# Kernel optimization log

Measured on AMD Instinct MI355X. Metric: run time of the kernel, lower is better.

Reference implementation:

```python
import jax, jax.numpy as jnp
import numpy as np

B, D, U1, U2 = 16384, 512, 512, 512
BN_EPS = 1e-3  # keras BatchNormalization default epsilon


def sparsemax(z):
    # z: [..., D]; standard sparsemax along last axis (Martins & Astudillo)
    d = z.shape[-1]
    z_sorted = -jnp.sort(-z, axis=-1)                      # descending
    z_cum = jnp.cumsum(z_sorted, axis=-1)
    k = jnp.arange(1, d + 1, dtype=z.dtype)
    support = (1.0 + k * z_sorted) > z_cum                 # [..., D] bool
    k_z = jnp.sum(support, axis=-1, keepdims=True)         # support size
    tau = (jnp.take_along_axis(z_cum, k_z.astype(jnp.int32) - 1, axis=-1) - 1.0) / k_z.astype(z.dtype)
    return jnp.maximum(z - tau, 0.0)


def setup_inputs() -> dict:
    key = jax.random.key(0)
    ks = jax.random.split(key, 8)
    x = jax.random.normal(ks[0], (B, D), dtype=jnp.float32)
    W1 = jax.random.normal(ks[1], (D, U1), dtype=jnp.float32) * 0.05
    b1 = jnp.zeros((U1,), jnp.float32)
    centers = jax.random.normal(ks[2], (U2, D), dtype=jnp.float32)      # paraboloid centers
    coefs = jax.random.normal(ks[3], (U2, D), dtype=jnp.float32) * 0.1  # paraboloid axis coefficients
    bn_gamma = jnp.ones((D,), jnp.float32)
    bn_beta = jnp.zeros((D,), jnp.float32)
    bn_mean = jnp.zeros((D,), jnp.float32)
    bn_var = jnp.ones((D,), jnp.float32)
    W_out = jax.random.normal(ks[4], (U1 + U2, D), dtype=jnp.float32) * 0.05
    b_out = jnp.zeros((D,), jnp.float32)
    w_add = jnp.array([0.5, 0.5], jnp.float32)  # WeightedAdd learnable scalars
    return {"x": x, "W1": W1, "b1": b1, "centers": centers, "coefs": coefs,
            "bn_gamma": bn_gamma, "bn_beta": bn_beta, "bn_mean": bn_mean, "bn_var": bn_var,
            "W_out": W_out, "b_out": b_out, "w_add": w_add}


def reference(x, W1, b1, centers, coefs, bn_gamma, bn_beta, bn_mean, bn_var, W_out, b_out, w_add):
    # Dense branch
    h1 = jax.nn.relu(x @ W1 + b1)                               # [B, U1]
    # BoundedParaboloids branch: BatchNorm (inference stats) then bounded paraboloids
    xb = (x - bn_mean) * jax.lax.rsqrt(bn_var + BN_EPS) * bn_gamma + bn_beta
    # q_j = sum_d (coefs[j,d] * (xb_d - centers[j,d]))^2, computed via GEMMs
    A = coefs * coefs                                            # [U2, D]
    q = (xb * xb) @ A.T - 2.0 * (xb @ (A * centers).T) + jnp.sum(A * centers * centers, axis=-1)
    h2 = jax.nn.relu(1.0 - q)                                    # [B, U2] bounded paraboloids
    # Output embedding: Dense(relu) on concat
    emb = jax.nn.relu(jnp.concatenate([h1, h2], axis=-1) @ W_out + b_out)  # [B, D]
    # WeightedAdd of (dropout-identity) inputs and embedding; dropout_rate=0 / inference
    pre = w_add[0] * x + w_add[1] * emb
    mask = sparsemax(pre)                                        # [B, D]
    return mask
```

## Files before the change

kernel.cpp:

```cpp
#include <hip/hip_runtime.h>
#include <math.h>

typedef float f4 __attribute__((ext_vector_type(4)));
typedef float f32x4 __attribute__((ext_vector_type(4)));
typedef __bf16 bf16x8 __attribute__((ext_vector_type(8)));
typedef unsigned short u16;
typedef u16 us8 __attribute__((ext_vector_type(8)));

__device__ __forceinline__ u16 f2bf(float f) {
  unsigned u = __builtin_bit_cast(unsigned, f);
  unsigned r = u + 0x7fffu + ((u >> 16) & 1u);
  return (u16)(r >> 16);
}
__device__ __forceinline__ float bf2f(u16 h) {
  unsigned u = ((unsigned)h) << 16;
  return __builtin_bit_cast(float, u);
}

__global__ __launch_bounds__(256) void prep_bn_kernel(
    const float* __restrict__ gamma, const float* __restrict__ beta,
    const float* __restrict__ mean, const float* __restrict__ var,
    float* __restrict__ scale, float* __restrict__ shift) {
  int d = blockIdx.x * blockDim.x + threadIdx.x;
  if (d < 512) {
    float s = rsqrtf(var[d] + 1e-3f) * gamma[d];
    scale[d] = s;
    shift[d] = beta[d] - mean[d] * s;
  }
}

__global__ __launch_bounds__(64) void prep_params_kernel(
    const float* __restrict__ coefs, const float* __restrict__ centers,
    u16* __restrict__ pth, float* __restrict__ cvec) {
  int j = blockIdx.x;
  int l = threadIdx.x;
  int d0 = l * 8;
  f4 c0 = *(const f4*)(coefs + (size_t)j * 512 + d0);
  f4 c1 = *(const f4*)(coefs + (size_t)j * 512 + d0 + 4);
  f4 e0 = *(const f4*)(centers + (size_t)j * 512 + d0);
  f4 e1 = *(const f4*)(centers + (size_t)j * 512 + d0 + 4);
  us8 pa, pb;
  float acc = 0.f;
#pragma unroll
  for (int e = 0; e < 8; ++e) {
    float cf = (e < 4) ? c0[e] : c1[e - 4];
    float ce = (e < 4) ? e0[e] : e1[e - 4];
    float a = cf * cf;
    pa[e] = f2bf(a);
    pb[e] = f2bf(-2.f * a * ce);
    acc = fmaf(a * ce, ce, acc);
  }
  *(us8*)(pth + (size_t)j * 1024 + d0) = pa;
  *(us8*)(pth + (size_t)j * 1024 + 512 + d0) = pb;
#pragma unroll
  for (int off = 32; off; off >>= 1) acc += __shfl_xor(acc, off);
  if (l == 0) cvec[j] = acc;
}

__global__ __launch_bounds__(256) void transpose_split_kernel(
    const float* __restrict__ in, u16* __restrict__ th, u16* __restrict__ tl,
    int K, int N) {
  __shared__ float t[32][33];
  int lx = threadIdx.x;
  int ly = threadIdx.y;
  int n0 = blockIdx.x * 32, k0 = blockIdx.y * 32;
#pragma unroll
  for (int i = 0; i < 4; ++i)
    t[ly + 8 * i][lx] = in[(size_t)(k0 + ly + 8 * i) * N + n0 + lx];
  __syncthreads();
#pragma unroll
  for (int i = 0; i < 4; ++i) {
    float v = t[lx][ly + 8 * i];
    u16 h = f2bf(v);
    u16 lo = f2bf(v - bf2f(h));
    th[(size_t)(n0 + ly + 8 * i) * K + k0 + lx] = h;
    tl[(size_t)(n0 + ly + 8 * i) * K + k0 + lx] = lo;
  }
}

__global__ __launch_bounds__(256) void conv_x_kernel(
    const float* __restrict__ x, const float* __restrict__ scale,
    const float* __restrict__ shift, u16* __restrict__ xh,
    u16* __restrict__ xb) {
  int gid = blockIdx.x * 256 + threadIdx.x;
  int m = gid >> 6;
  int d0 = (gid & 63) * 8;
  f4 v0 = *(const f4*)(x + (size_t)m * 512 + d0);
  f4 v1 = *(const f4*)(x + (size_t)m * 512 + d0 + 4);
  f4 s0 = *(const f4*)(scale + d0);
  f4 s1 = *(const f4*)(scale + d0 + 4);
  f4 h0 = *(const f4*)(shift + d0);
  f4 h1 = *(const f4*)(shift + d0 + 4);
  us8 oh, ob;
#pragma unroll
  for (int e = 0; e < 8; ++e) {
    float xv = (e < 4) ? v0[e] : v1[e - 4];
    float sc = (e < 4) ? s0[e] : s1[e - 4];
    float sh = (e < 4) ? h0[e] : h1[e - 4];
    oh[e] = f2bf(xv);
    ob[e] = f2bf(fmaf(xv, sc, sh));
  }
  *(us8*)(xh + (size_t)m * 512 + d0) = oh;
  *(us8*)(xb + (size_t)m * 512 + d0) = ob;
}

template <int MODE, int PASSES>
__global__ __launch_bounds__(256, 2) void gemm_mfma(
    const u16* __restrict__ Ah, const u16* __restrict__ Bh,
    const u16* __restrict__ Bl, const float* __restrict__ bias,
    const float* __restrict__ xorig, const float* __restrict__ wadd,
    u16* __restrict__ Hout, float* __restrict__ outp, int K, int lda,
    int coff) {
  extern __shared__ char smem[];
  char* sA = smem;
  char* sBh = smem + 16384;
  char* sBl = smem + 32768;
  const int tid = threadIdx.x;
  const int l = tid & 63;
  const int w = tid >> 6;
  const int wm = w & 1, wn = w >> 1;
  const int lr = l & 15, lk = l >> 4;
  const int sx = lr & 7;
  const int bid = blockIdx.x;
  const int lin = (bid & 7) * 64 + (bid >> 3);
  const int m0 = (lin >> 2) * 128, n0 = (lin & 3) * 128;
  const int srow = l >> 3;
  const int sslot = (l & 7) ^ srow;

  f32x4 acc[4][4];
#pragma unroll
  for (int i = 0; i < 4; ++i)
#pragma unroll
    for (int j = 0; j < 4; ++j) acc[i][j] = (f32x4){0.f, 0.f, 0.f, 0.f};

  for (int k0 = 0; k0 < K; k0 += 64) {
#pragma unroll
    for (int p = 0; p < 4; ++p) {
      int c = p * 4 + w;
      int row = c * 8 + srow;
      int loff = c * 1024;
      size_t gob = (size_t)(n0 + row) * K + k0 + sslot * 8;
      __builtin_amdgcn_global_load_lds(
          (const __attribute__((address_space(1))) void*)(Bh + gob),
          (__attribute__((address_space(3))) void*)(sBh + loff), 16, 0, 0);
      if (PASSES == 2) {
        __builtin_amdgcn_global_load_lds(
            (const __attribute__((address_space(1))) void*)(Bl + gob),
            (__attribute__((address_space(3))) void*)(sBl + loff), 16, 0, 0);
      }
      if (MODE == 2) {
        int kb = (k0 < 512) ? k0 : (k0 - 512);
        us8 v = *(const us8*)(Ah + (size_t)(m0 + row) * 512 + kb + sslot * 8);
        us8 o;
        if (k0 < 512) {
#pragma unroll
          for (int e = 0; e < 8; ++e) {
            float f = bf2f(v[e]);
            o[e] = f2bf(f * f);
          }
        } else {
          o = v;
        }
        *(us8*)(sA + loff + l * 16) = o;
      } else {
        size_t goa = (size_t)(m0 + row) * lda + k0 + sslot * 8;
        __builtin_amdgcn_global_load_lds(
            (const __attribute__((address_space(1))) void*)(Ah + goa),
            (__attribute__((address_space(3))) void*)(sA + loff), 16, 0, 0);
      }
    }
    __syncthreads();
#pragma unroll
    for (int ks = 0; ks < 2; ++ks) {
      bf16x8 av[4], bv[4];
#pragma unroll
      for (int i = 0; i < 4; ++i)
        av[i] = *(const bf16x8*)(sA + (wm * 64 + i * 16 + lr) * 128 +
                                 (((ks * 4 + lk) ^ sx) * 16));
#pragma unroll
      for (int j = 0; j < 4; ++j)
        bv[j] = *(const bf16x8*)(sBh + (wn * 64 + j * 16 + lr) * 128 +
                                 (((ks * 4 + lk) ^ sx) * 16));
#pragma unroll
      for (int i = 0; i < 4; ++i)
#pragma unroll
        for (int j = 0; j < 4; ++j)
          acc[i][j] = __builtin_amdgcn_mfma_f32_16x16x32_bf16(av[i], bv[j],
                                                              acc[i][j], 0, 0, 0);
      if (PASSES == 2) {
#pragma unroll
        for (int j = 0; j < 4; ++j)
          bv[j] = *(const bf16x8*)(sBl + (wn * 64 + j * 16 + lr) * 128 +
                                   (((ks * 4 + lk) ^ sx) * 16));
#pragma unroll
        for (int i = 0; i < 4; ++i)
#pragma unroll
          for (int j = 0; j < 4; ++j)
            acc[i][j] = __builtin_amdgcn_mfma_f32_16x16x32_bf16(
                av[i], bv[j], acc[i][j], 0, 0, 0);
      }
    }
    __syncthreads();
  }

  const int mwb = m0 + wm * 64;
  const int nwb = n0 + wn * 64;
  if (MODE == 3) {
    float w0 = wadd[0], w1 = wadd[1];
#pragma unroll
    for (int j = 0; j < 4; ++j) {
      int n = nwb + j * 16 + lr;
      float bv = bias[n];
#pragma unroll
      for (int i = 0; i < 4; ++i) {
#pragma unroll
        for (int r = 0; r < 4; ++r) {
          int m = mwb + i * 16 + lk * 4 + r;
          float v = fmaxf(acc[i][j][r] + bv, 0.f);
          outp[(size_t)m * 512 + n] =
              fmaf(w1, v, w0 * xorig[(size_t)m * 512 + n]);
        }
      }
    }
  } else {
#pragma unroll
    for (int j = 0; j < 4; ++j) {
      int n = nwb + j * 16 + lr;
      float bv = bias[n];
#pragma unroll
      for (int i = 0; i < 4; ++i) {
#pragma unroll
        for (int r = 0; r < 4; ++r) {
          int m = mwb + i * 16 + lk * 4 + r;
          float v = acc[i][j][r] + bv;
          v = (MODE == 1) ? fmaxf(v, 0.f) : fmaxf(1.f - v, 0.f);
          Hout[(size_t)m * 1024 + coff + n] = f2bf(v);
        }
      }
    }
  }
}

__global__ __launch_bounds__(256) void sparsemax_kernel(float* __restrict__ out) {
  int row = blockIdx.x * 4 + (threadIdx.x >> 6);
  int lane = threadIdx.x & 63;
  float* rp = out + (size_t)row * 512;
  f4 z0 = *(const f4*)(rp + lane * 8);
  f4 z1 = *(const f4*)(rp + lane * 8 + 4);
  float z[8];
#pragma unroll
  for (int e = 0; e < 4; ++e) {
    z[e] = z0[e];
    z[4 + e] = z1[e];
  }
  float m = z[0];
#pragma unroll
  for (int i = 1; i < 8; ++i) m = fmaxf(m, z[i]);
#pragma unroll
  for (int off = 32; off; off >>= 1) m = fmaxf(m, __shfl_xor(m, off));
  float tau = m - 1.0f;
  for (int it = 0; it < 32; ++it) {
    float s = 0.f, k = 0.f;
#pragma unroll
    for (int i = 0; i < 8; ++i) {
      if (z[i] > tau) {
        s += z[i] - tau;
        k += 1.f;
      }
    }
#pragma unroll
    for (int off = 32; off; off >>= 1) {
      s += __shfl_xor(s, off);
      k += __shfl_xor(k, off);
    }
    if (k < 0.5f) break;
    float tn = tau + (s - 1.f) / k;
    if (tn == tau) break;
    tau = tn;
  }
  float s = 0.f, k = 0.f;
#pragma unroll
  for (int i = 0; i < 8; ++i)
    if (z[i] > tau) {
      s += z[i];
      k += 1.f;
    }
#pragma unroll
  for (int off = 32; off; off >>= 1) {
    s += __shfl_xor(s, off);
    k += __shfl_xor(k, off);
  }
  float tauf = (k >= 0.5f) ? (s - 1.f) / k : (m - 1.f);
  f4 o0, o1;
#pragma unroll
  for (int e = 0; e < 4; ++e) {
    o0[e] = fmaxf(z[e] - tauf, 0.f);
    o1[e] = fmaxf(z[4 + e] - tauf, 0.f);
  }
  *(f4*)(rp + lane * 8) = o0;
  *(f4*)(rp + lane * 8 + 4) = o1;
}

extern "C" void kernel_launch(void* const* d_in, const int* in_sizes, int n_in,
                              void* d_out, int out_size, void* d_ws,
                              size_t ws_size, hipStream_t stream) {
  const float* x = (const float*)d_in[0];
  const float* W1 = (const float*)d_in[1];
  const float* b1 = (const float*)d_in[2];
  const float* centers = (const float*)d_in[3];
  const float* coefs = (const float*)d_in[4];
  const float* gamma = (const float*)d_in[5];
  const float* beta = (const float*)d_in[6];
  const float* mean = (const float*)d_in[7];
  const float* var = (const float*)d_in[8];
  const float* W_out = (const float*)d_in[9];
  const float* b_out = (const float*)d_in[10];
  const float* wadd = (const float*)d_in[11];
  float* out = (float*)d_out;

  char* ws = (char*)d_ws;
  u16* Hh = (u16*)(ws);
  u16* Xh = (u16*)(ws + 33554432);
  u16* Xb = (u16*)(ws + 50331648);
  char* pool = ws + 67108864;
  u16* W1th = (u16*)(pool);
  u16* W1tl = (u16*)(pool + 524288);
  u16* Pth = (u16*)(pool + 1048576);
  u16* Wth = (u16*)(pool);
  u16* Wtl = (u16*)(pool + 1048576);
  float* cvec = (float*)(ws + 69206016);
  float* scale = (float*)(ws + 69208064);
  float* shift = (float*)(ws + 69210112);

  prep_bn_kernel<<<2, 256, 0, stream>>>(gamma, beta, mean, var, scale, shift);
  prep_params_kernel<<<512, 64, 0, stream>>>(coefs, centers, Pth, cvec);
  transpose_split_kernel<<<dim3(16, 16), dim3(32, 8), 0, stream>>>(W1, W1th,
                                                                   W1tl, 512,
                                                                   512);
  conv_x_kernel<<<4096, 256, 0, stream>>>(x, scale, shift, Xh, Xb);

  gemm_mfma<1, 1><<<512, 256, 32768, stream>>>(Xh, W1th, nullptr, b1, nullptr,
                                               nullptr, Hh, nullptr, 512, 512,
                                               0);
  gemm_mfma<2, 1><<<512, 256, 32768, stream>>>(Xb, Pth, nullptr, cvec,
                                               nullptr, nullptr, Hh, nullptr,
                                               1024, 512, 512);
  transpose_split_kernel<<<dim3(16, 32), dim3(32, 8), 0, stream>>>(W_out, Wth,
                                                                   Wtl, 1024,
                                                                   512);
  gemm_mfma<3, 2><<<512, 256, 49152, stream>>>(Hh, Wth, Wtl, b_out, x, wadd,
                                               nullptr, out, 1024, 1024, 0);
  sparsemax_kernel<<<4096, 256, 0, stream>>>(out);
}
```

Baseline: 128.1 us.

## Fuse dense and paraboloid GEMMs into one launch; drop lo pass for h2

The two first-stage GEMMs (dense branch with K=512 and paraboloid branch with K=1024) now run as a single launch of 1024 blocks. Each block picks its branch from its block index, and the occupancy hint is raised to 4 blocks per CU. This removes one launch and its tail and lets both branches fill the GPU together. The output GEMM also now applies the bf16 hi/lo split of W_out only for the first 512 K entries (the h1 half), cutting matrix-core work and LDS traffic, at some cost in precision on the h2 contribution.

```diff
diff --git a/kernel.cpp b/kernel.cpp
--- a/kernel.cpp
+++ b/kernel.cpp
@@ -104,13 +104,116 @@
   *(us8*)(xb + (size_t)m * 512 + d0) = ob;
 }
 
-template <int MODE, int PASSES>
-__global__ __launch_bounds__(256, 2) void gemm_mfma(
+__global__ __launch_bounds__(256, 4) void gemm_fused12(
+    const u16* __restrict__ Xh, const u16* __restrict__ Xb,
+    const u16* __restrict__ W1th, const u16* __restrict__ Pth,
+    const float* __restrict__ b1, const float* __restrict__ cvec,
+    u16* __restrict__ Hout) {
+  extern __shared__ char smem[];
+  char* sA = smem;
+  char* sBh = smem + 16384;
+  const int tid = threadIdx.x;
+  const int l = tid & 63;
+  const int w = tid >> 6;
+  const int wm = w & 1, wn = w >> 1;
+  const int lr = l & 15, lk = l >> 4;
+  const int sx = lr & 7;
+  const int bid = blockIdx.x;
+  const int L = (bid & 7) * 128 + (bid >> 3);
+  const int p = L >> 3;
+  const int g = (L >> 2) & 1;
+  const int n = L & 3;
+  const int m0 = p * 128, n0 = n * 128;
+  const int Kg = g ? 1024 : 512;
+  const u16* Bmat = g ? Pth : W1th;
+  const u16* Amat = g ? Xb : Xh;
+  const int srow = l >> 3;
+  const int sslot = (l & 7) ^ srow;
+
+  f32x4 acc[4][4];
+#pragma unroll
+  for (int i = 0; i < 4; ++i)
+#pragma unroll
+    for (int j = 0; j < 4; ++j) acc[i][j] = (f32x4){0.f, 0.f, 0.f, 0.f};
+
+  for (int k0 = 0; k0 < Kg; k0 += 64) {
+#pragma unroll
+    for (int pp = 0; pp < 4; ++pp) {
+      int c = pp * 4 + w;
+      int row = c * 8 + srow;
+      int loff = c * 1024;
+      size_t gob = (size_t)(n0 + row) * Kg + k0 + sslot * 8;
+      __builtin_amdgcn_global_load_lds(
+          (const __attribute__((address_space(1))) void*)(Bmat + gob),
+          (__attribute__((address_space(3))) void*)(sBh + loff), 16, 0, 0);
+      if (g) {
+        int kb = (k0 < 512) ? k0 : (k0 - 512);
+        us8 v = *(const us8*)(Amat + (size_t)(m0 + row) * 512 + kb + sslot * 8);
+        us8 o;
+        if (k0 < 512) {
+#pragma unroll
+          for (int e = 0; e < 8; ++e) {
+            float f = bf2f(v[e]);
+            o[e] = f2bf(f * f);
+          }
+        } else {
+          o = v;
+        }
+        *(us8*)(sA + loff + l * 16) = o;
+      } else {
+        size_t goa = (size_t)(m0 + row) * 512 + k0 + sslot * 8;
+        __builtin_amdgcn_global_load_lds(
+            (const __attribute__((address_space(1))) void*)(Amat + goa),
+            (__attribute__((address_space(3))) void*)(sA + loff), 16, 0, 0);
+      }
+    }
+    __syncthreads();
+#pragma unroll
+    for (int ks = 0; ks < 2; ++ks) {
+      bf16x8 av[4], bv[4];
+#pragma unroll
+      for (int i = 0; i < 4; ++i)
+        av[i] = *(const bf16x8*)(sA + (wm * 64 + i * 16 + lr) * 128 +
+                                 (((ks * 4 + lk) ^ sx) * 16));
+#pragma unroll
+      for (int j = 0; j < 4; ++j)
+        bv[j] = *(const bf16x8*)(sBh + (wn * 64 + j * 16 + lr) * 128 +
+                                 (((ks * 4 + lk) ^ sx) * 16));
+#pragma unroll
+      for (int i = 0; i < 4; ++i)
+#pragma unroll
+        for (int j = 0; j < 4; ++j)
+          acc[i][j] = __builtin_amdgcn_mfma_f32_16x16x32_bf16(av[i], bv[j],
+                                                              acc[i][j], 0, 0, 0);
+    }
+    __syncthreads();
+  }
+
+  const int mwb = m0 + wm * 64;
+  const int nwb = n0 + wn * 64;
+  const float* bias = g ? cvec : b1;
+#pragma unroll
+  for (int j = 0; j < 4; ++j) {
+    int nn = nwb + j * 16 + lr;
+    float bv = bias[nn];
+#pragma unroll
+    for (int i = 0; i < 4; ++i) {
+#pragma unroll
+      for (int r = 0; r < 4; ++r) {
+        int m = mwb + i * 16 + lk * 4 + r;
+        float v = acc[i][j][r] + bv;
+        v = g ? fmaxf(1.f - v, 0.f) : fmaxf(v, 0.f);
+        Hout[(size_t)m * 1024 + g * 512 + nn] = f2bf(v);
+      }
+    }
+  }
+}
+
+__global__ __launch_bounds__(256, 2) void gemm3(
     const u16* __restrict__ Ah, const u16* __restrict__ Bh,
     const u16* __restrict__ Bl, const float* __restrict__ bias,
     const float* __restrict__ xorig, const float* __restrict__ wadd,
-    u16* __restrict__ Hout, float* __restrict__ outp, int K, int lda,
-    int coff) {
+    float* __restrict__ outp) {
   extern __shared__ char smem[];
   char* sA = smem;
   char* sBh = smem + 16384;
@@ -133,41 +236,26 @@
 #pragma unroll
     for (int j = 0; j < 4; ++j) acc[i][j] = (f32x4){0.f, 0.f, 0.f, 0.f};
 
-  for (int k0 = 0; k0 < K; k0 += 64) {
-#pragma unroll
-    for (int p = 0; p < 4; ++p) {
-      int c = p * 4 + w;
+  for (int k0 = 0; k0 < 1024; k0 += 64) {
+    const bool lo = (k0 < 512);
+#pragma unroll
+    for (int pp = 0; pp < 4; ++pp) {
+      int c = pp * 4 + w;
       int row = c * 8 + srow;
       int loff = c * 1024;
-      size_t gob = (size_t)(n0 + row) * K + k0 + sslot * 8;
+      size_t gob = (size_t)(n0 + row) * 1024 + k0 + sslot * 8;
+      size_t goa = (size_t)(m0 + row) * 1024 + k0 + sslot * 8;
       __builtin_amdgcn_global_load_lds(
           (const __attribute__((address_space(1))) void*)(Bh + gob),
           (__attribute__((address_space(3))) void*)(sBh + loff), 16, 0, 0);
-      if (PASSES == 2) {
+      __builtin_amdgcn_global_load_lds(
+          (const __attribute__((address_space(1))) void*)(Ah + goa),
+          (__attribute__((address_space(3))) void*)(sA + loff), 16, 0, 0);
+      if (lo) {
         __builtin_amdgcn_global_load_lds(
             (const __attribute__((address_space(1))) void*)(Bl + gob),
             (__attribute__((address_space(3))) void*)(sBl + loff), 16, 0, 0);
       }
-      if (MODE == 2) {
-        int kb = (k0 < 512) ? k0 : (k0 - 512);
-        us8 v = *(const us8*)(Ah + (size_t)(m0 + row) * 512 + kb + sslot * 8);
-        us8 o;
-        if (k0 < 512) {
-#pragma unroll
-          for (int e = 0; e < 8; ++e) {
-            float f = bf2f(v[e]);
-            o[e] = f2bf(f * f);
-          }
-        } else {
-          o = v;
-        }
-        *(us8*)(sA + loff + l * 16) = o;
-      } else {
-        size_t goa = (size_t)(m0 + row) * lda + k0 + sslot * 8;
-        __builtin_amdgcn_global_load_lds(
-            (const __attribute__((address_space(1))) void*)(Ah + goa),
-            (__attribute__((address_space(3))) void*)(sA + loff), 16, 0, 0);
-      }
     }
     __syncthreads();
 #pragma unroll
@@ -187,7 +275,7 @@
         for (int j = 0; j < 4; ++j)
           acc[i][j] = __builtin_amdgcn_mfma_f32_16x16x32_bf16(av[i], bv[j],
                                                               acc[i][j], 0, 0, 0);
-      if (PASSES == 2) {
+      if (lo) {
 #pragma unroll
         for (int j = 0; j < 4; ++j)
           bv[j] = *(const bf16x8*)(sBl + (wn * 64 + j * 16 + lr) * 128 +
@@ -205,37 +293,18 @@
 
   const int mwb = m0 + wm * 64;
   const int nwb = n0 + wn * 64;
-  if (MODE == 3) {
-    float w0 = wadd[0], w1 = wadd[1];
-#pragma unroll
-    for (int j = 0; j < 4; ++j) {
-      int n = nwb + j * 16 + lr;
-      float bv = bias[n];
-#pragma unroll
-      for (int i = 0; i < 4; ++i) {
-#pragma unroll
-        for (int r = 0; r < 4; ++r) {
-          int m = mwb + i * 16 + lk * 4 + r;
-          float v = fmaxf(acc[i][j][r] + bv, 0.f);
-          outp[(size_t)m * 512 + n] =
-              fmaf(w1, v, w0 * xorig[(size_t)m * 512 + n]);
-        }
-      }
-    }
-  } else {
-#pragma unroll
-    for (int j = 0; j < 4; ++j) {
-      int n = nwb + j * 16 + lr;
-      float bv = bias[n];
-#pragma unroll
-      for (int i = 0; i < 4; ++i) {
-#pragma unroll
-        for (int r = 0; r < 4; ++r) {
-          int m = mwb + i * 16 + lk * 4 + r;
-          float v = acc[i][j][r] + bv;
-          v = (MODE == 1) ? fmaxf(v, 0.f) : fmaxf(1.f - v, 0.f);
-          Hout[(size_t)m * 1024 + coff + n] = f2bf(v);
-        }
+  float w0 = wadd[0], w1 = wadd[1];
+#pragma unroll
+  for (int j = 0; j < 4; ++j) {
+    int n = nwb + j * 16 + lr;
+    float bv = bias[n];
+#pragma unroll
+    for (int i = 0; i < 4; ++i) {
+#pragma unroll
+      for (int r = 0; r < 4; ++r) {
+        int m = mwb + i * 16 + lk * 4 + r;
+        float v = fmaxf(acc[i][j][r] + bv, 0.f);
+        outp[(size_t)m * 512 + n] = fmaf(w1, v, w0 * xorig[(size_t)m * 512 + n]);
       }
     }
   }
@@ -339,16 +408,11 @@
                                                                    512);
   conv_x_kernel<<<4096, 256, 0, stream>>>(x, scale, shift, Xh, Xb);
 
-  gemm_mfma<1, 1><<<512, 256, 32768, stream>>>(Xh, W1th, nullptr, b1, nullptr,
-                                               nullptr, Hh, nullptr, 512, 512,
-                                               0);
-  gemm_mfma<2, 1><<<512, 256, 32768, stream>>>(Xb, Pth, nullptr, cvec,
-                                               nullptr, nullptr, Hh, nullptr,
-                                               1024, 512, 512);
+  gemm_fused12<<<1024, 256, 32768, stream>>>(Xh, Xb, W1th, Pth, b1, cvec, Hh);
+
   transpose_split_kernel<<<dim3(16, 32), dim3(32, 8), 0, stream>>>(W_out, Wth,
                                                                    Wtl, 1024,
                                                                    512);
-  gemm_mfma<3, 2><<<512, 256, 49152, stream>>>(Hh, Wth, Wtl, b_out, x, wadd,
-                                               nullptr, out, 1024, 1024, 0);
+  gemm3<<<512, 256, 49152, stream>>>(Hh, Wth, Wtl, b_out, x, wadd, out);
   sparsemax_kernel<<<4096, 256, 0, stream>>>(out);
 }
```

New measurement: 122.3 us. 1.05x faster.
